# Optimization experiments

Measured on AMD Instinct MI355X. Metric: run time of the kernel, lower is better.

Reference implementation:

```python
import jax, jax.numpy as jnp
import numpy as np

D, H, K, L, F, G, M, OUT = 1280, 16, 80, 4, 5120, 48, 2, 2048
HALF = K // 2  # rotary half dim = 40


def _token_coords(grid_thw, merge_size, N):
    tpi = grid_thw[:, 0] * grid_thw[:, 1] * grid_thw[:, 2]
    cu = jnp.concatenate([jnp.zeros(1, jnp.int32), jnp.cumsum(tpi).astype(jnp.int32)])
    tok = jnp.arange(N, dtype=jnp.int32)
    img_id = jnp.searchsorted(cu[1:], tok, side='right')
    local = tok - cu[img_id]
    h = grid_thw[img_id, 1]
    w = grid_thw[img_id, 2]
    spatial = local % (h * w)
    msq = merge_size * merge_size
    mw = w // merge_size
    group, intra = spatial // msq, spatial % msq
    row = (group // mw) * merge_size + intra // merge_size
    col = (group % mw) * merge_size + intra % merge_size
    return row, col, h, w, cu


def _layernorm(x, s, b, eps=1e-6):
    mu = jnp.mean(x, -1, keepdims=True)
    var = jnp.mean(jnp.square(x - mu), -1, keepdims=True)
    return (x - mu) * jax.lax.rsqrt(var + eps) * s + b


def _rotate_half(x):
    x1, x2 = x[..., :HALF], x[..., HALF:]
    return jnp.concatenate([-x2, x1], axis=-1)


def setup_inputs() -> dict:
    key = jax.random.key(0)
    ks = jax.random.split(key, 16)
    s = 0.02
    inp = {
        'pixels': jax.random.normal(ks[0], (2048, 1536), jnp.float32),
        'grid_thw': jnp.array([[1, 16, 32]] * 4, jnp.int32),
        'pos_embed': jax.random.normal(ks[1], (G * G, D), jnp.float32) * s,
        'patch_w': jax.random.normal(ks[2], (1536, D), jnp.float32) * s,
        'patch_b': jnp.zeros((D,), jnp.float32),
        'ln1_s': jnp.ones((L, D), jnp.float32), 'ln1_b': jnp.zeros((L, D), jnp.float32),
        'qkv_w': jax.random.normal(ks[3], (L, D, 3 * D), jnp.float32) * s,
        'qkv_b': jnp.zeros((L, 3 * D), jnp.float32),
        'proj_w': jax.random.normal(ks[4], (L, D, D), jnp.float32) * s,
        'proj_b': jnp.zeros((L, D), jnp.float32),
        'ln2_s': jnp.ones((L, D), jnp.float32), 'ln2_b': jnp.zeros((L, D), jnp.float32),
        'fc1_w': jax.random.normal(ks[5], (L, D, F), jnp.float32) * s,
        'fc1_b': jnp.zeros((L, F), jnp.float32),
        'fc2_w': jax.random.normal(ks[6], (L, F, D), jnp.float32) * s,
        'fc2_b': jnp.zeros((L, D), jnp.float32),
        'm_norm_s': jnp.ones((D,), jnp.float32), 'm_norm_b': jnp.zeros((D,), jnp.float32),
        'm_fc1_w': jax.random.normal(ks[7], (D * M * M, D * M * M), jnp.float32) * s,
        'm_fc1_b': jnp.zeros((D * M * M,), jnp.float32),
        'm_fc2_w': jax.random.normal(ks[8], (D * M * M, OUT), jnp.float32) * s,
        'm_fc2_b': jnp.zeros((OUT,), jnp.float32),
    }
    return inp


def _forward(pixels, grid_thw, pos_embed, patch_w, patch_b, ln1_s, ln1_b, qkv_w, qkv_b,
             proj_w, proj_b, ln2_s, ln2_b, fc1_w, fc1_b, fc2_w, fc2_b,
             m_norm_s, m_norm_b, m_fc1_w, m_fc1_b, m_fc2_w, m_fc2_b):
    N = pixels.shape[0]
    row, col, h, w, cu = _token_coords(grid_thw, M, N)

    # patch embed: conv with stride==kernel over flattened patches == linear
    x = pixels @ patch_w + patch_b  # [N, D]

    # bilinear position-embedding interpolation onto each image's (h, w) grid
    rf = jnp.where(h > 1, row.astype(jnp.float32) * (G - 1) / jnp.maximum(h - 1, 1), 0.0)
    cf = jnp.where(w > 1, col.astype(jnp.float32) * (G - 1) / jnp.maximum(w - 1, 1), 0.0)
    r0 = jnp.floor(rf).astype(jnp.int32); r1 = jnp.minimum(r0 + 1, G - 1)
    c0 = jnp.floor(cf).astype(jnp.int32); c1 = jnp.minimum(c0 + 1, G - 1)
    wr = (rf - r0)[:, None]; wc = (cf - c0)[:, None]
    pe = (pos_embed[r0 * G + c0] * (1 - wr) * (1 - wc)
          + pos_embed[r0 * G + c1] * (1 - wr) * wc
          + pos_embed[r1 * G + c0] * wr * (1 - wc)
          + pos_embed[r1 * G + c1] * wr * wc)
    x = x + pe

    # 2-D rotary embeddings
    inv_freq = 1.0 / (10000.0 ** (jnp.arange(0, HALF, 2, dtype=jnp.float32) / HALF))
    freqs = jnp.concatenate([row[:, None].astype(jnp.float32) * inv_freq,
                             col[:, None].astype(jnp.float32) * inv_freq], axis=-1)  # [N, HALF]
    emb = jnp.concatenate([freqs, freqs], axis=-1)  # [N, K]
    cos, sin = jnp.cos(emb)[:, None, :], jnp.sin(emb)[:, None, :]  # [N,1,K]

    # block-diagonal segment mask via cu_seqlens (N is a multiple of 128; no pad)
    tok = jnp.arange(N)
    seg = jnp.searchsorted(cu[1:], tok, side='right')
    k_start = cu[jnp.minimum(seg, cu.shape[0] - 2)]
    k_end = cu[jnp.minimum(seg + 1, cu.shape[0] - 1)]
    mask = (tok[None, :] >= k_start[:, None]) & (tok[None, :] < k_end[:, None])  # [N,N]
    scale = K ** -0.5

    for l in range(L):
        hdn = _layernorm(x, ln1_s[l], ln1_b[l])
        qkv = (hdn @ qkv_w[l] + qkv_b[l]).reshape(N, 3, H, K)
        q, k, v = qkv[:, 0], qkv[:, 1], qkv[:, 2]
        q = q * cos + _rotate_half(q) * sin
        k = k * cos + _rotate_half(k) * sin
        scores = jnp.einsum('nhk,mhk->hnm', q, k) * scale
        scores = jnp.where(mask[None], scores, jnp.finfo(scores.dtype).min)
        attn = jax.nn.softmax(scores, axis=-1)
        o = jnp.einsum('hnm,mhk->nhk', attn, v).reshape(N, D)
        x = x + o @ proj_w[l] + proj_b[l]

        hdn = _layernorm(x, ln2_s[l], ln2_b[l])
        ff = jax.nn.gelu(hdn @ fc1_w[l] + fc1_b[l], approximate=True)
        x = x + ff @ fc2_w[l] + fc2_b[l]

    # patch merger
    normed = _layernorm(x, m_norm_s, m_norm_b).reshape(N // (M * M), D * M * M)
    ff = jax.nn.gelu(normed @ m_fc1_w + m_fc1_b, approximate=True)
    return ff @ m_fc2_w + m_fc2_b  # [N/4, OUT]


def reference(pixels, grid_thw, pos_embed, patch_w, patch_b, ln1_s, ln1_b, qkv_w, qkv_b,
              proj_w, proj_b, ln2_s, ln2_b, fc1_w, fc1_b, fc2_w, fc2_b,
              m_norm_s, m_norm_b, m_fc1_w, m_fc1_b, m_fc2_w, m_fc2_b):
    return _forward(pixels, grid_thw, pos_embed, patch_w, patch_b, ln1_s, ln1_b, qkv_w, qkv_b,
                    proj_w, proj_b, ln2_s, ln2_b, fc1_w, fc1_b, fc2_w, fc2_b,
                    m_norm_s, m_norm_b, m_fc1_w, m_fc1_b, m_fc2_w, m_fc2_b)
```

## Files before the change

kernel.cpp:

```cpp
#include <hip/hip_runtime.h>
#include <math.h>

#define DMODEL 1280
#define NHEADS 16
#define FDIM   5120
#define GPOS   48
#define SEG    512

typedef __attribute__((ext_vector_type(8))) short bf16x8;
typedef __attribute__((ext_vector_type(4))) float f32x4;
typedef unsigned short u16;

__device__ __forceinline__ u16 f2bf(float f) {
  unsigned int u = __float_as_uint(f);
  u = (u + 0x7FFFu + ((u >> 16) & 1u)) >> 16;
  return (u16)u;
}
__device__ __forceinline__ float bf2f(u16 u) {
  return __uint_as_float((unsigned int)u << 16);
}
__device__ __forceinline__ float gelu_tanh(float x) {
  float u = 0.7978845608028654f * (x + 0.044715f * x * x * x);
  float t = __expf(2.f * u);
  float th = 1.f - 2.f / (t + 1.f);
  return 0.5f * x * (1.f + th);
}

typedef const __attribute__((address_space(1))) unsigned int* gas_t;
typedef __attribute__((address_space(3))) unsigned int* las_t;
__device__ __forceinline__ void async16(const void* g, void* l) {
  __builtin_amdgcn_global_load_lds((gas_t)g, (las_t)l, 16, 0, 0);
}

#define STG256(mat, PW, ldx, h, kk, pp)                          \
  do {                                                           \
    const u16* g_ = (PW) + (long long)(h) * 128 * (ldx) + (kk);  \
    async16(g_, &L[pp][mat][h][(w * 2 + 0) * 512]);              \
    async16(g_ + 32, &L[pp][mat][h][(w * 2 + 1) * 512]);         \
  } while (0)

#define MM256(ii, ff)                                                          \
  acc[ii][ff] = __builtin_amdgcn_mfma_f32_16x16x32_bf16(aR[(ii) & 3][0],       \
                    bR[ff][0], acc[ii][ff], 0, 0, 0);                          \
  acc[ii][ff] = __builtin_amdgcn_mfma_f32_16x16x32_bf16(aR[(ii) & 3][1],       \
                    bR[ff][1], acc[ii][ff], 0, 0, 0);

#define BAR256() asm volatile("s_barrier" ::: "memory")
#define LGKM0() asm volatile("s_waitcnt lgkmcnt(0)" ::: "memory")

template <int EPI>
__global__ __launch_bounds__(512, 2) void gemm256(
    const u16* __restrict__ A, const u16* __restrict__ B,
    const float* __restrict__ bias, void* __restrict__ Cv,
    int Kd, int lda, int ldb, int ldc, int nsplit, long long pstride) {
  __shared__ __align__(16) u16 L[2][2][2][8192];
  const int sp = blockIdx.z;
  const int Ks = Kd / nsplit;
  const int NT = Ks >> 6;
  const u16* Ab = A + (long long)sp * Ks;
  const u16* Bb = B + (long long)sp * Ks;
  const int m0 = blockIdx.x * 256, n0 = blockIdx.y * 256;
  const int t = threadIdx.x, ln = t & 63, w = t >> 6;
  const int wr = w >> 2, wc = w & 3;
  const int m16 = ln & 15, q = ln >> 4;
  const int r16 = ln >> 2;
  const int csw = (ln & 3) ^ ((ln >> 5) << 1);
  const int rbase = m16 * 32 + (q ^ ((m16 >> 3) << 1)) * 8;

  const u16* Aw = Ab + (long long)(m0 + w * 16 + r16) * lda + csw * 8;
  const u16* Bw = Bb + (long long)(n0 + w * 16 + r16) * ldb + csw * 8;

  f32x4 acc[8][4];
#pragma unroll
  for (int i = 0; i < 8; i++)
#pragma unroll
    for (int j = 0; j < 4; j++)
#pragma unroll
      for (int r = 0; r < 4; r++) acc[i][j][r] = 0.f;

  STG256(0, Aw, lda, 0, 0, 0);
  STG256(0, Aw, lda, 1, 0, 0);
  STG256(1, Bw, ldb, 0, 0, 0);
  STG256(1, Bw, ldb, 1, 0, 0);
  if (NT > 1) {
    STG256(1, Bw, ldb, 0, 64, 1);
    STG256(1, Bw, ldb, 1, 64, 1);
    asm volatile("s_waitcnt vmcnt(4)" ::: "memory");
  } else {
    asm volatile("s_waitcnt vmcnt(0)" ::: "memory");
  }
  BAR256();

  const int wb = (wc & 1) * 4;
  for (int tt = 0; tt < NT; ++tt) {
    const int p = tt & 1;
    const u16* Abuf = &L[p][0][wr][0];
    const u16* Bbuf = &L[p][1][wc >> 1][0];
    bf16x8 aR[4][2], bR[4][2];

#pragma unroll
    for (int i = 0; i < 4; ++i) {
      aR[i][0] = *(const bf16x8*)(Abuf + (i * 2 + 0) * 512 + rbase);
      aR[i][1] = *(const bf16x8*)(Abuf + (i * 2 + 1) * 512 + rbase);
    }
#pragma unroll
    for (int fc = 0; fc < 2; ++fc) {
      bR[fc][0] = *(const bf16x8*)(Bbuf + ((wb + fc) * 2 + 0) * 512 + rbase);
      bR[fc][1] = *(const bf16x8*)(Bbuf + ((wb + fc) * 2 + 1) * 512 + rbase);
    }
    if (tt + 1 < NT) STG256(0, Aw, lda, 0, (tt + 1) * 64, (tt + 1) & 1);
    BAR256();
    LGKM0();
    __builtin_amdgcn_s_setprio(1);
#pragma unroll
    for (int i = 0; i < 4; ++i) { MM256(i, 0); MM256(i, 1); }
    __builtin_amdgcn_s_setprio(0);
    BAR256();

#pragma unroll
    for (int fc = 2; fc < 4; ++fc) {
      bR[fc][0] = *(const bf16x8*)(Bbuf + ((wb + fc) * 2 + 0) * 512 + rbase);
      bR[fc][1] = *(const bf16x8*)(Bbuf + ((wb + fc) * 2 + 1) * 512 + rbase);
    }
    if (tt + 1 < NT) STG256(0, Aw, lda, 1, (tt + 1) * 64, (tt + 1) & 1);
    BAR256();
    LGKM0();
    __builtin_amdgcn_s_setprio(1);
#pragma unroll
    for (int i = 0; i < 4; ++i) { MM256(i, 2); MM256(i, 3); }
    __builtin_amdgcn_s_setprio(0);
    BAR256();

#pragma unroll
    for (int i = 0; i < 4; ++i) {
      aR[i][0] = *(const bf16x8*)(Abuf + ((4 + i) * 2 + 0) * 512 + rbase);
      aR[i][1] = *(const bf16x8*)(Abuf + ((4 + i) * 2 + 1) * 512 + rbase);
    }
    if (tt + 2 < NT) STG256(1, Bw, ldb, 0, (tt + 2) * 64, p);
    BAR256();
    LGKM0();
    __builtin_amdgcn_s_setprio(1);
#pragma unroll
    for (int i = 0; i < 4; ++i) { MM256(4 + i, 2); MM256(4 + i, 3); }
    __builtin_amdgcn_s_setprio(0);
    BAR256();

    if (tt + 2 < NT) STG256(1, Bw, ldb, 1, (tt + 2) * 64, p);
    BAR256();
    LGKM0();
    __builtin_amdgcn_s_setprio(1);
#pragma unroll
    for (int i = 0; i < 4; ++i) { MM256(4 + i, 0); MM256(4 + i, 1); }
    __builtin_amdgcn_s_setprio(0);
    if (tt + 1 < NT) {
      if (tt + 2 < NT) asm volatile("s_waitcnt vmcnt(4)" ::: "memory");
      else             asm volatile("s_waitcnt vmcnt(0)" ::: "memory");
    }
    BAR256();
  }

#pragma unroll
  for (int fr = 0; fr < 8; fr++) {
#pragma unroll
    for (int r = 0; r < 4; r++) {
      int row = m0 + wr * 128 + fr * 16 + q * 4 + r;
      if (EPI == 0) {
        u16* Cp = (u16*)Cv + (long long)sp * pstride + (long long)row * ldc;
#pragma unroll
        for (int fc = 0; fc < 4; fc++)
          Cp[n0 + wc * 64 + fc * 16 + m16] = f2bf(acc[fr][fc][r]);
      } else if (EPI == 1) {
        u16* Cb = (u16*)Cv + (long long)row * ldc;
#pragma unroll
        for (int fc = 0; fc < 4; fc++) {
          int col = n0 + wc * 64 + fc * 16 + m16;
          Cb[col] = f2bf(acc[fr][fc][r] + bias[col]);
        }
      } else {
        u16* Cb = (u16*)Cv + (long long)row * ldc;
#pragma unroll
        for (int fc = 0; fc < 4; fc++) {
          int col = n0 + wc * 64 + fc * 16 + m16;
          Cb[col] = f2bf(gelu_tanh(acc[fr][fc][r] + bias[col]));
        }
      }
    }
  }
}

__global__ __launch_bounds__(256) void fattn_k(
    const u16* __restrict__ qr, const u16* __restrict__ kr,
    const u16* __restrict__ vpT, u16* __restrict__ o, int N, float iscale) {
  __shared__ __align__(16) u16 Ks[2][24][512];
  __shared__ __align__(16) u16 Vs[2][20][512];
  __shared__ __align__(16) u16 Ps[4][32 * 128];
  const int nseg = N >> 9;
  const int hb = blockIdx.y;
  const int h = hb / nseg, seg = hb - h * nseg;
  const int t = threadIdx.x, ln = t & 63, w = t >> 6;
  const int m16 = ln & 15, qh = ln >> 4;
  const int r4 = ln >> 2, gsw = (ln & 3) ^ ((ln >> 5) << 1);
  const int rbase = m16 * 32 + ((qh ^ ((m16 >> 3) << 1)) << 3);
  const long long hN = (long long)h * N;
  const int segbase = seg * SEG;
  const int q0 = segbase + blockIdx.x * 128 + w * 32;

  bf16x8 qf[2][3];
#pragma unroll
  for (int mi = 0; mi < 2; mi++)
#pragma unroll
    for (int ks = 0; ks < 3; ks++)
      qf[mi][ks] = *(const bf16x8*)&qr[(hN + q0 + mi * 16 + m16) * 96 + ks * 32 + qh * 8];

  f32x4 ao[2][5];
#pragma unroll
  for (int mi = 0; mi < 2; mi++)
#pragma unroll
    for (int df = 0; df < 5; df++)
#pragma unroll
      for (int r = 0; r < 4; r++) ao[mi][df][r] = 0.f;
  float m_[2][4], l_[2][4];
#pragma unroll
  for (int mi = 0; mi < 2; mi++)
#pragma unroll
    for (int r = 0; r < 4; r++) { m_[mi][r] = -1e30f; l_[mi][r] = 0.f; }

  auto stage = [&](int c, int pb) {
#pragma unroll
    for (int i = 0; i < 6; i++) {
      int sK = w * 6 + i, f = sK / 3, kg = sK - f * 3;
      async16(&kr[(hN + segbase + c * 128 + f * 16 + r4) * 96 + kg * 32 + gsw * 8],
              &Ks[pb][sK][0]);
    }
#pragma unroll
    for (int i = 0; i < 5; i++) {
      int sV = w * 5 + i, df = sV >> 2, kvg = sV & 3;
      async16(&vpT[((long long)hb * 128 + df * 16 + r4) * SEG + c * 128 + kvg * 32 + gsw * 8],
              &Vs[pb][sV][0]);
    }
  };

  stage(0, 0);
  u16* Pmy = &Ps[w][0];
  for (int c = 0; c < 4; c++) {
    const int pb = c & 1;
    __syncthreads();
    if (c < 3) stage(c + 1, pb ^ 1);

    f32x4 s[2][8];
#pragma unroll
    for (int mi = 0; mi < 2; mi++)
#pragma unroll
      for (int f = 0; f < 8; f++)
#pragma unroll
        for (int r = 0; r < 4; r++) s[mi][f][r] = 0.f;
#pragma unroll
    for (int ks = 0; ks < 3; ks++) {
#pragma unroll
      for (int f = 0; f < 8; f++) {
        bf16x8 kf = *(const bf16x8*)&Ks[pb][f * 3 + ks][rbase];
#pragma unroll
        for (int mi = 0; mi < 2; mi++)
          s[mi][f] = __builtin_amdgcn_mfma_f32_16x16x32_bf16(qf[mi][ks], kf, s[mi][f], 0, 0, 0);
      }
    }

#pragma unroll
    for (int mi = 0; mi < 2; mi++) {
#pragma unroll
      for (int r = 0; r < 4; r++) {
        float mx = s[mi][0][r];
#pragma unroll
        for (int f = 1; f < 8; f++) mx = fmaxf(mx, s[mi][f][r]);
        mx *= iscale;
#pragma unroll
        for (int o2 = 1; o2 <= 8; o2 <<= 1) mx = fmaxf(mx, __shfl_xor(mx, o2));
        float mn = fmaxf(m_[mi][r], mx);
        float corr = __expf(m_[mi][r] - mn);
        m_[mi][r] = mn;
        float rs = 0.f;
#pragma unroll
        for (int f = 0; f < 8; f++) {
          float p = __expf(s[mi][f][r] * iscale - mn);
          s[mi][f][r] = p;
          rs += p;
        }
#pragma unroll
        for (int o2 = 1; o2 <= 8; o2 <<= 1) rs += __shfl_xor(rs, o2);
        l_[mi][r] = l_[mi][r] * corr + rs;
#pragma unroll
        for (int df = 0; df < 5; df++) ao[mi][df][r] *= corr;
      }
    }

#pragma unroll
    for (int mi = 0; mi < 2; mi++) {
#pragma unroll
      for (int r = 0; r < 4; r++) {
        int qq = mi * 16 + qh * 4 + r;
        int base = qq * 128 + (m16 & 7);
        int ql = qq & 7;
#pragma unroll
        for (int f = 0; f < 8; f++) {
          int gr = (f * 2 + (m16 >> 3)) ^ ql;
          Pmy[base + gr * 8] = f2bf(s[mi][f][r]);
        }
      }
    }

#pragma unroll
    for (int ks = 0; ks < 4; ks++) {
      bf16x8 pf[2];
#pragma unroll
      for (int mi = 0; mi < 2; mi++)
        pf[mi] = *(const bf16x8*)&Pmy[(mi * 16 + m16) * 128 +
                                      (((ks * 4 + qh) ^ (m16 & 7)) << 3)];
#pragma unroll
      for (int df = 0; df < 5; df++) {
        bf16x8 vf = *(const bf16x8*)&Vs[pb][df * 4 + ks][rbase];
#pragma unroll
        for (int mi = 0; mi < 2; mi++)
          ao[mi][df] = __builtin_amdgcn_mfma_f32_16x16x32_bf16(pf[mi], vf, ao[mi][df], 0, 0, 0);
      }
    }
  }

#pragma unroll
  for (int mi = 0; mi < 2; mi++) {
#pragma unroll
    for (int r = 0; r < 4; r++) {
      float rl = 1.f / l_[mi][r];
      long long rowb = (long long)(q0 + mi * 16 + qh * 4 + r) * DMODEL + h * 80;
#pragma unroll
      for (int df = 0; df < 5; df++)
        o[rowb + df * 16 + m16] = f2bf(ao[mi][df][r] * rl);
    }
  }
}

template <int S, int RES, int GELU, int OUTBF>
__global__ void reduce_k(const u16* __restrict__ Pp, long long mn, int Nn,
                         const float* __restrict__ bias,
                         const float* __restrict__ res, void* __restrict__ out) {
  long long i = ((long long)blockIdx.x * 256 + threadIdx.x) * 4;
  if (i >= mn) return;
  float vx = 0.f, vy = 0.f, vz = 0.f, vw = 0.f;
#pragma unroll
  for (int s = 0; s < S; s++) {
    ushort4 u4 = *(const ushort4*)(Pp + (long long)s * mn + i);
    vx += bf2f(u4.x); vy += bf2f(u4.y); vz += bf2f(u4.z); vw += bf2f(u4.w);
  }
  int col = (int)(i % Nn);
  vx += bias[col]; vy += bias[col + 1]; vz += bias[col + 2]; vw += bias[col + 3];
  if (GELU) {
    vx = gelu_tanh(vx); vy = gelu_tanh(vy);
    vz = gelu_tanh(vz); vw = gelu_tanh(vw);
  }
  if (RES) {
    float4 r4 = *(const float4*)(res + i);
    vx += r4.x; vy += r4.y; vz += r4.z; vw += r4.w;
  }
  if (OUTBF) {
    ushort4 o; o.x = f2bf(vx); o.y = f2bf(vy); o.z = f2bf(vz); o.w = f2bf(vw);
    *(ushort4*)((u16*)out + i) = o;
  } else {
    float4 o; o.x = vx; o.y = vy; o.z = vz; o.w = vw;
    *(float4*)((float*)out + i) = o;
  }
}

template <int S>
__global__ void redln_k(const u16* __restrict__ Pp, long long mn,
                        const float* __restrict__ bias,
                        float* __restrict__ x,
                        const float* __restrict__ s, const float* __restrict__ b,
                        u16* __restrict__ h) {
  int row = blockIdx.x;
  int d = threadIdx.x * 4;
  long long base = (long long)row * DMODEL + d;
  float vx = 0.f, vy = 0.f, vz = 0.f, vw = 0.f;
#pragma unroll
  for (int si = 0; si < S; si++) {
    ushort4 u4 = *(const ushort4*)(Pp + (long long)si * mn + base);
    vx += bf2f(u4.x); vy += bf2f(u4.y); vz += bf2f(u4.z); vw += bf2f(u4.w);
  }
  vx += bias[d]; vy += bias[d + 1]; vz += bias[d + 2]; vw += bias[d + 3];
  float4 r4 = *(const float4*)(x + base);
  vx += r4.x; vy += r4.y; vz += r4.z; vw += r4.w;
  float4 xv; xv.x = vx; xv.y = vy; xv.z = vz; xv.w = vw;
  *(float4*)(x + base) = xv;
  float sum = vx + vy + vz + vw;
#pragma unroll
  for (int o = 32; o; o >>= 1) sum += __shfl_xor(sum, o);
  __shared__ float red[8];
  int wv = threadIdx.x >> 6, lnn = threadIdx.x & 63;
  if (lnn == 0) red[wv] = sum;
  __syncthreads();
  float mu = 0.f;
  for (int i = 0; i < 5; i++) mu += red[i];
  mu *= (1.f / DMODEL);
  float dx = vx - mu, dy = vy - mu, dz = vz - mu, dw = vw - mu;
  float s2 = dx * dx + dy * dy + dz * dz + dw * dw;
#pragma unroll
  for (int o = 32; o; o >>= 1) s2 += __shfl_xor(s2, o);
  __syncthreads();
  if (lnn == 0) red[wv] = s2;
  __syncthreads();
  float var = 0.f;
  for (int i = 0; i < 5; i++) var += red[i];
  var *= (1.f / DMODEL);
  float rs = rsqrtf(var + 1e-6f);
  ushort4 o4;
  o4.x = f2bf(dx * rs * s[d] + b[d]);
  o4.y = f2bf(dy * rs * s[d + 1] + b[d + 1]);
  o4.z = f2bf(dz * rs * s[d + 2] + b[d + 2]);
  o4.w = f2bf(dw * rs * s[d + 3] + b[d + 3]);
  *(ushort4*)(h + base) = o4;
}

__global__ void wconv_k(const float* __restrict__ in, u16* __restrict__ out,
                        int K, int N) {
  __shared__ float tl[32][33];
  int n0 = blockIdx.x * 32, k0 = blockIdx.y * 32;
  int t = threadIdx.x;
  int r = t >> 5, c = t & 31;
#pragma unroll
  for (int i = 0; i < 4; i++)
    tl[r + 8 * i][c] = in[(long long)(k0 + r + 8 * i) * N + n0 + c];
  __syncthreads();
  int n = t >> 4, kp = (t & 15) * 2;
#pragma unroll
  for (int i = 0; i < 2; i++) {
    ushort2 o;
    o.x = f2bf(tl[kp][n + 16 * i]);
    o.y = f2bf(tl[kp + 1][n + 16 * i]);
    *(ushort2*)&out[(long long)(n0 + n + 16 * i) * K + k0 + kp] = o;
  }
}

__global__ void conv_k(const float* __restrict__ in, u16* __restrict__ out,
                       long long n) {
  long long i = ((long long)blockIdx.x * 256 + threadIdx.x) * 4;
  if (i >= n) return;
  float4 v = *(const float4*)(in + i);
  ushort4 o; o.x = f2bf(v.x); o.y = f2bf(v.y); o.z = f2bf(v.z); o.w = f2bf(v.w);
  *(ushort4*)&out[i] = o;
}

union U16x8 { uint4 v; u16 s[8]; };
__global__ void vtr_k(const u16* __restrict__ in, u16* __restrict__ out) {
  __shared__ u16 tl[64][65];
  int b = blockIdx.z;
  int m0 = blockIdx.x * 64;
  int d0 = blockIdx.y * 64;
  const u16* ib = in + (long long)b * SEG * 128;
  u16* ob = out + (long long)b * 128 * SEG;
  int t = threadIdx.x;
  int r = t >> 3, c8 = (t & 7) * 8;
#pragma unroll
  for (int i = 0; i < 2; i++) {
    U16x8 ld;
    ld.v = *(const uint4*)&ib[(long long)(m0 + r + 32 * i) * 128 + d0 + c8];
#pragma unroll
    for (int j = 0; j < 8; j++) tl[r + 32 * i][c8 + j] = ld.s[j];
  }
  __syncthreads();
  int d = t >> 3, m8 = (t & 7) * 8;
#pragma unroll
  for (int i = 0; i < 2; i++) {
    int dd = d + 32 * i;
    U16x8 st;
#pragma unroll
    for (int j = 0; j < 8; j++) st.s[j] = tl[m8 + j][dd];
    *(uint4*)&ob[(long long)(d0 + dd) * SEG + m0 + m8] = st.v;
  }
}

__global__ void coords_k(const int* __restrict__ g, int nimg,
                         int* __restrict__ rw, int* __restrict__ cl,
                         int* __restrict__ hh, int* __restrict__ ww, int N) {
  int t = blockIdx.x * 256 + threadIdx.x;
  if (t >= N) return;
  int c = 0, local = 0, H = 1, W = 1;
  for (int i = 0; i < nimg; i++) {
    int tpi = g[i * 3] * g[i * 3 + 1] * g[i * 3 + 2];
    if (t >= c && t < c + tpi) { local = t - c; H = g[i * 3 + 1]; W = g[i * 3 + 2]; }
    c += tpi;
  }
  int hw = H * W;
  int sp = local % hw;
  int mw = W >> 1;
  int gr = sp >> 2, intra = sp & 3;
  rw[t] = (gr / mw) * 2 + (intra >> 1);
  cl[t] = (gr % mw) * 2 + (intra & 1);
  hh[t] = H; ww[t] = W;
}

__global__ void peadd_k(float* __restrict__ x, const float* __restrict__ pe,
                        const int* __restrict__ rw, const int* __restrict__ cl,
                        const int* __restrict__ hh, const int* __restrict__ ww) {
  int n = blockIdx.x;
  int d = threadIdx.x * 4;
  int H = hh[n], W = ww[n];
  float rf = (H > 1) ? (float)rw[n] * (float)(GPOS - 1) / (float)(H - 1) : 0.f;
  float cf = (W > 1) ? (float)cl[n] * (float)(GPOS - 1) / (float)(W - 1) : 0.f;
  int r0 = (int)floorf(rf), c0 = (int)floorf(cf);
  int r1 = min(r0 + 1, GPOS - 1), c1 = min(c0 + 1, GPOS - 1);
  float wr = rf - (float)r0, wc = cf - (float)c0;
  float w00 = (1.f - wr) * (1.f - wc), w01 = (1.f - wr) * wc;
  float w10 = wr * (1.f - wc), w11 = wr * wc;
  float4 v00 = *(const float4*)(pe + (long long)(r0 * GPOS + c0) * DMODEL + d);
  float4 v01 = *(const float4*)(pe + (long long)(r0 * GPOS + c1) * DMODEL + d);
  float4 v10 = *(const float4*)(pe + (long long)(r1 * GPOS + c0) * DMODEL + d);
  float4 v11 = *(const float4*)(pe + (long long)(r1 * GPOS + c1) * DMODEL + d);
  float4 xv = *(float4*)(x + (long long)n * DMODEL + d);
  xv.x += w00 * v00.x + w01 * v01.x + w10 * v10.x + w11 * v11.x;
  xv.y += w00 * v00.y + w01 * v01.y + w10 * v10.y + w11 * v11.y;
  xv.z += w00 * v00.z + w01 * v01.z + w10 * v10.z + w11 * v11.z;
  xv.w += w00 * v00.w + w01 * v01.w + w10 * v10.w + w11 * v11.w;
  *(float4*)(x + (long long)n * DMODEL + d) = xv;
}

__global__ void ln_k(const float* __restrict__ X, u16* __restrict__ Y,
                     const float* __restrict__ s, const float* __restrict__ b) {
  int row = blockIdx.x;
  int d = threadIdx.x * 4;
  const float* x = X + (long long)row * DMODEL;
  float4 v = *(const float4*)(x + d);
  float sum = v.x + v.y + v.z + v.w;
#pragma unroll
  for (int o = 32; o; o >>= 1) sum += __shfl_xor(sum, o);
  __shared__ float red[8];
  int wv = threadIdx.x >> 6, lnn = threadIdx.x & 63;
  if (lnn == 0) red[wv] = sum;
  __syncthreads();
  float mu = 0.f;
  for (int i = 0; i < 5; i++) mu += red[i];
  mu *= (1.f / DMODEL);
  float dx = v.x - mu, dy = v.y - mu, dz = v.z - mu, dw = v.w - mu;
  float s2 = dx * dx + dy * dy + dz * dz + dw * dw;
#pragma unroll
  for (int o = 32; o; o >>= 1) s2 += __shfl_xor(s2, o);
  __syncthreads();
  if (lnn == 0) red[wv] = s2;
  __syncthreads();
  float var = 0.f;
  for (int i = 0; i < 5; i++) var += red[i];
  var *= (1.f / DMODEL);
  float rs = rsqrtf(var + 1e-6f);
  ushort4 o4;
  o4.x = f2bf(dx * rs * s[d] + b[d]);
  o4.y = f2bf(dy * rs * s[d + 1] + b[d + 1]);
  o4.z = f2bf(dz * rs * s[d + 2] + b[d + 2]);
  o4.w = f2bf(dw * rs * s[d + 3] + b[d + 3]);
  *(ushort4*)(Y + (long long)row * DMODEL + d) = o4;
}

__global__ void rope_k(const u16* __restrict__ qkv, const int* __restrict__ rw,
                       const int* __restrict__ cl, u16* __restrict__ qr,
                       u16* __restrict__ kr, u16* __restrict__ vp, int N) {
  int n = blockIdx.x, h = blockIdx.y, t = threadIdx.x;
  const u16* src = qkv + (long long)n * (3 * DMODEL) + h * 80;
  long long ob96 = ((long long)h * N + n) * 96;
  long long ob128 = ((long long)h * N + n) * 128;
  if (t < 40) {
    float pos = (t < 20) ? (float)rw[n] : (float)cl[n];
    float infr = exp2f(-13.287712379549449f * (float)(t % 20) * 0.05f);
    float f = pos * infr;
    float cs = cosf(f), sn = sinf(f);
    float q0 = bf2f(src[t]), q1 = bf2f(src[t + 40]);
    qr[ob96 + t] = f2bf(q0 * cs - q1 * sn);
    qr[ob96 + t + 40] = f2bf(q1 * cs + q0 * sn);
    float k0 = bf2f(src[DMODEL + t]), k1 = bf2f(src[DMODEL + t + 40]);
    kr[ob96 + t] = f2bf(k0 * cs - k1 * sn);
    kr[ob96 + t + 40] = f2bf(k1 * cs + k0 * sn);
    vp[ob128 + t] = src[2 * DMODEL + t];
    vp[ob128 + t + 40] = src[2 * DMODEL + t + 40];
  } else {
    int u = t - 40;
    if (u < 16) { qr[ob96 + 80 + u] = 0; kr[ob96 + 80 + u] = 0; }
    vp[ob128 + 80 + u] = 0;
    vp[ob128 + 104 + u] = 0;
  }
}

static void gemm_big(hipStream_t st, int epi, const u16* A, const u16* B,
                     const float* bias, void* C, int M, int Nn, int Kd,
                     int lda, int ldb, int ldc, int nsplit) {
  dim3 g(M / 256, Nn / 256, nsplit), blk(512);
  long long ps = (long long)M * Nn;
  switch (epi) {
    case 0: gemm256<0><<<g, blk, 0, st>>>(A, B, bias, C, Kd, lda, ldb, ldc, nsplit, ps); break;
    case 1: gemm256<1><<<g, blk, 0, st>>>(A, B, bias, C, Kd, lda, ldb, ldc, nsplit, ps); break;
    default: gemm256<3><<<g, blk, 0, st>>>(A, B, bias, C, Kd, lda, ldb, ldc, nsplit, ps); break;
  }
}

extern "C" void kernel_launch(void* const* d_in, const int* in_sizes, int n_in,
                              void* d_out, int out_size, void* d_ws, size_t ws_size,
                              hipStream_t stream) {
  const float* pixels = (const float*)d_in[0];
  const int* grid_thw = (const int*)d_in[1];
  const float* pos_embed = (const float*)d_in[2];
  const float* patch_w = (const float*)d_in[3];
  const float* patch_b = (const float*)d_in[4];
  const float* ln1_s = (const float*)d_in[5];
  const float* ln1_b = (const float*)d_in[6];
  const float* qkv_w = (const float*)d_in[7];
  const float* qkv_b = (const float*)d_in[8];
  const float* proj_w = (const float*)d_in[9];
  const float* proj_b = (const float*)d_in[10];
  const float* ln2_s = (const float*)d_in[11];
  const float* ln2_b = (const float*)d_in[12];
  const float* fc1_w = (const float*)d_in[13];
  const float* fc1_b = (const float*)d_in[14];
  const float* fc2_w = (const float*)d_in[15];
  const float* fc2_b = (const float*)d_in[16];
  const float* mns = (const float*)d_in[17];
  const float* mnb = (const float*)d_in[18];
  const float* mf1w = (const float*)d_in[19];
  const float* mf1b = (const float*)d_in[20];
  const float* mf2w = (const float*)d_in[21];
  const float* mf2b = (const float*)d_in[22];
  float* out = (float*)d_out;

  const int N = in_sizes[0] / 1536;
  const int nimg = in_sizes[1] / 3;
  const int nseg = N / SEG;
  const int nb = NHEADS * nseg;

  char* w = (char*)d_ws;
  size_t off = 0;
  auto alloc = [&](size_t bytes) -> void* {
    void* p = w + off;
    off += (bytes + 255) & ~(size_t)255;
    return p;
  };
  int* rw = (int*)alloc((size_t)N * 4);
  int* cl = (int*)alloc((size_t)N * 4);
  int* hh = (int*)alloc((size_t)N * 4);
  int* ww = (int*)alloc((size_t)N * 4);
  float* x = (float*)alloc((size_t)N * DMODEL * 4);
  u16* h = (u16*)alloc((size_t)N * DMODEL * 2);
  u16* pixbf = (u16*)alloc((size_t)N * 1536 * 2);
  u16* patchT = (u16*)alloc((size_t)DMODEL * 1536 * 2);
  u16* qkvT = (u16*)alloc((size_t)3 * DMODEL * DMODEL * 2);
  u16* projT = (u16*)alloc((size_t)DMODEL * DMODEL * 2);
  u16* fc1T = (u16*)alloc((size_t)FDIM * DMODEL * 2);
  u16* fc2T = (u16*)alloc((size_t)DMODEL * FDIM * 2);
  u16* qkvb = (u16*)alloc((size_t)N * 3 * DMODEL * 2);
  u16* qr = (u16*)alloc((size_t)NHEADS * N * 96 * 2);
  u16* kr = (u16*)alloc((size_t)NHEADS * N * 96 * 2);
  u16* vp = (u16*)alloc((size_t)NHEADS * N * 128 * 2);
  u16* vpT = (u16*)alloc((size_t)NHEADS * N * 128 * 2);
  u16* pad0 = (u16*)alloc((size_t)nb * 2 * SEG * 128 * 2);
  u16* o = (u16*)alloc((size_t)N * DMODEL * 2);
  float* bigA = (float*)alloc((size_t)nb * SEG * SEG * 4);
  float* bigB = (float*)alloc((size_t)nb * SEG * SEG * 2);
  (void)ws_size; (void)pad0;
  u16* mfc1T = qkvb;
  u16* mfc2T = pixbf;
  u16* ffb = (u16*)bigA;
  u16* mf = (u16*)bigA;
  u16* part = (u16*)bigB;
  u16* partA = (u16*)bigA + (size_t)11 * 1024 * 1024;

  const float iscale = 0.11180339887498949f;
  const long long mnD = (long long)N * DMODEL;

  coords_k<<<dim3((N + 255) / 256), 256, 0, stream>>>(grid_thw, nimg, rw, cl, hh, ww, N);
  conv_k<<<dim3((int)(((long long)N * 1536 / 4 + 255) / 256)), 256, 0, stream>>>(
      pixels, pixbf, (long long)N * 1536);
  wconv_k<<<dim3(DMODEL / 32, 1536 / 32), 256, 0, stream>>>(patch_w, patchT, 1536, DMODEL);
  gemm_big(stream, 0, pixbf, patchT, nullptr, part, N, DMODEL, 1536, 1536, 1536,
           DMODEL, 4);
  reduce_k<4, 0, 0, 0><<<dim3((int)((mnD / 4 + 255) / 256)), 256, 0, stream>>>(
      part, mnD, DMODEL, patch_b, nullptr, x);
  peadd_k<<<dim3(N), 320, 0, stream>>>(x, pos_embed, rw, cl, hh, ww);
  ln_k<<<dim3(N), 320, 0, stream>>>(x, h, ln1_s, ln1_b);

  for (int l = 0; l < 4; l++) {
    wconv_k<<<dim3(3 * DMODEL / 32, DMODEL / 32), 256, 0, stream>>>(
        qkv_w + (size_t)l * DMODEL * 3 * DMODEL, qkvT, DMODEL, 3 * DMODEL);
    wconv_k<<<dim3(DMODEL / 32, DMODEL / 32), 256, 0, stream>>>(
        proj_w + (size_t)l * DMODEL * DMODEL, projT, DMODEL, DMODEL);
    wconv_k<<<dim3(FDIM / 32, DMODEL / 32), 256, 0, stream>>>(
        fc1_w + (size_t)l * DMODEL * FDIM, fc1T, DMODEL, FDIM);
    wconv_k<<<dim3(DMODEL / 32, FDIM / 32), 256, 0, stream>>>(
        fc2_w + (size_t)l * FDIM * DMODEL, fc2T, FDIM, DMODEL);

    gemm_big(stream, 0, h, qkvT, nullptr, part, N, 3 * DMODEL, DMODEL,
             DMODEL, DMODEL, 3 * DMODEL, 2);
    reduce_k<2, 0, 0, 1><<<dim3((int)(((long long)N * 3 * DMODEL / 4 + 255) / 256)), 256, 0, stream>>>(
        part, (long long)N * 3 * DMODEL, 3 * DMODEL,
        qkv_b + (size_t)l * 3 * DMODEL, nullptr, qkvb);
    rope_k<<<dim3(N, NHEADS), 64, 0, stream>>>(qkvb, rw, cl, qr, kr, vp, N);
    vtr_k<<<dim3(8, 2, nb), 256, 0, stream>>>(vp, vpT);
    fattn_k<<<dim3(SEG / 128, nb), 256, 0, stream>>>(qr, kr, vpT, o, N, iscale);
    gemm_big(stream, 0, o, projT, nullptr, part, N, DMODEL, DMODEL, DMODEL,
             DMODEL, DMODEL, 4);
    redln_k<4><<<dim3(N), 320, 0, stream>>>(part, mnD, proj_b + (size_t)l * DMODEL,
                                            x, ln2_s + (size_t)l * DMODEL,
                                            ln2_b + (size_t)l * DMODEL, h);
    gemm_big(stream, 0, h, fc1T, nullptr, partA, N, FDIM, DMODEL,
             DMODEL, DMODEL, FDIM, 2);
    reduce_k<2, 0, 1, 1><<<dim3((int)(((long long)N * FDIM / 4 + 255) / 256)), 256, 0, stream>>>(
        partA, (long long)N * FDIM, FDIM, fc1_b + (size_t)l * FDIM, nullptr, ffb);
    gemm_big(stream, 0, ffb, fc2T, nullptr, partA, N, DMODEL, FDIM, FDIM, FDIM,
             DMODEL, 8);
    const float* nsl = (l < 3) ? ln1_s + (size_t)(l + 1) * DMODEL : mns;
    const float* nbl = (l < 3) ? ln1_b + (size_t)(l + 1) * DMODEL : mnb;
    redln_k<8><<<dim3(N), 320, 0, stream>>>(partA, mnD, fc2_b + (size_t)l * DMODEL,
                                            x, nsl, nbl, h);
  }

  const int Mm = N / 4;
  wconv_k<<<dim3(FDIM / 32, FDIM / 32), 256, 0, stream>>>(mf1w, mfc1T, FDIM, FDIM);
  gemm_big(stream, 0, h, mfc1T, nullptr, partA, Mm, FDIM, FDIM, FDIM, FDIM, FDIM, 8);
  reduce_k<8, 0, 1, 1><<<dim3((int)(((long long)Mm * FDIM / 4 + 255) / 256)), 256, 0, stream>>>(
      partA, (long long)Mm * FDIM, FDIM, mf1b, nullptr, mf);
  wconv_k<<<dim3(2048 / 32, FDIM / 32), 256, 0, stream>>>(mf2w, mfc2T, FDIM, 2048);
  gemm_big(stream, 0, mf, mfc2T, nullptr, part, Mm, 2048, FDIM, FDIM, FDIM, 2048, 16);
  reduce_k<16, 0, 0, 0><<<dim3((int)(((long long)Mm * 2048 / 4 + 255) / 256)), 256, 0, stream>>>(
      part, (long long)Mm * 2048, 2048, mf2b, nullptr, out);
}
```

Baseline: 1.518 ms.

## Fuse bias epilogues into GEMMs, drop split-K for QKV/FC1, remap blocks across XCDs

```diff
diff --git a/kernel.cpp b/kernel.cpp
--- a/kernel.cpp
+++ b/kernel.cpp
@@ -30,6 +30,11 @@
 typedef __attribute__((address_space(3))) unsigned int* las_t;
 __device__ __forceinline__ void async16(const void* g, void* l) {
   __builtin_amdgcn_global_load_lds((gas_t)g, (las_t)l, 16, 0, 0);
+}
+
+__device__ __forceinline__ int xcd_remap(int b, int nwg) {
+  int q = nwg >> 3, r = nwg & 7, x = b & 7, d = b >> 3;
+  return (x < r ? x * (q + 1) : r * (q + 1) + (x - r) * q) + d;
 }
 
 #define STG256(mat, PW, ldx, h, kk, pp)                          \
@@ -59,7 +64,9 @@
   const int NT = Ks >> 6;
   const u16* Ab = A + (long long)sp * Ks;
   const u16* Bb = B + (long long)sp * Ks;
-  const int m0 = blockIdx.x * 256, n0 = blockIdx.y * 256;
+  const int gx = gridDim.x;
+  const int lg = xcd_remap(blockIdx.x + gx * blockIdx.y, gx * gridDim.y);
+  const int m0 = (lg % gx) * 256, n0 = (lg / gx) * 256;
   const int t = threadIdx.x, ln = t & 63, w = t >> 6;
   const int wr = w >> 2, wc = w & 3;
   const int m16 = ln & 15, q = ln >> 4;
@@ -195,7 +202,9 @@
   __shared__ __align__(16) u16 Vs[2][20][512];
   __shared__ __align__(16) u16 Ps[4][32 * 128];
   const int nseg = N >> 9;
-  const int hb = blockIdx.y;
+  const int gx = gridDim.x;
+  const int lg = xcd_remap(blockIdx.x + gx * blockIdx.y, gx * gridDim.y);
+  const int strip = lg % gx, hb = lg / gx;
   const int h = hb / nseg, seg = hb - h * nseg;
   const int t = threadIdx.x, ln = t & 63, w = t >> 6;
   const int m16 = ln & 15, qh = ln >> 4;
@@ -203,7 +212,7 @@
   const int rbase = m16 * 32 + ((qh ^ ((m16 >> 3) << 1)) << 3);
   const long long hN = (long long)h * N;
   const int segbase = seg * SEG;
-  const int q0 = segbase + blockIdx.x * 128 + w * 32;
+  const int q0 = segbase + strip * 128 + w * 32;
 
   bf16x8 qf[2][3];
 #pragma unroll
@@ -663,7 +672,6 @@
   u16* ffb = (u16*)bigA;
   u16* mf = (u16*)bigA;
   u16* part = (u16*)bigB;
-  u16* partA = (u16*)bigA + (size_t)11 * 1024 * 1024;
 
   const float iscale = 0.11180339887498949f;
   const long long mnD = (long long)N * DMODEL;
@@ -689,11 +697,8 @@
     wconv_k<<<dim3(DMODEL / 32, FDIM / 32), 256, 0, stream>>>(
         fc2_w + (size_t)l * FDIM * DMODEL, fc2T, FDIM, DMODEL);
 
-    gemm_big(stream, 0, h, qkvT, nullptr, part, N, 3 * DMODEL, DMODEL,
-             DMODEL, DMODEL, 3 * DMODEL, 2);
-    reduce_k<2, 0, 0, 1><<<dim3((int)(((long long)N * 3 * DMODEL / 4 + 255) / 256)), 256, 0, stream>>>(
-        part, (long long)N * 3 * DMODEL, 3 * DMODEL,
-        qkv_b + (size_t)l * 3 * DMODEL, nullptr, qkvb);
+    gemm_big(stream, 1, h, qkvT, qkv_b + (size_t)l * 3 * DMODEL, qkvb, N,
+             3 * DMODEL, DMODEL, DMODEL, DMODEL, 3 * DMODEL, 1);
     rope_k<<<dim3(N, NHEADS), 64, 0, stream>>>(qkvb, rw, cl, qr, kr, vp, N);
     vtr_k<<<dim3(8, 2, nb), 256, 0, stream>>>(vp, vpT);
     fattn_k<<<dim3(SEG / 128, nb), 256, 0, stream>>>(qr, kr, vpT, o, N, iscale);
@@ -702,23 +707,21 @@
     redln_k<4><<<dim3(N), 320, 0, stream>>>(part, mnD, proj_b + (size_t)l * DMODEL,
                                             x, ln2_s + (size_t)l * DMODEL,
                                             ln2_b + (size_t)l * DMODEL, h);
-    gemm_big(stream, 0, h, fc1T, nullptr, partA, N, FDIM, DMODEL,
-             DMODEL, DMODEL, FDIM, 2);
-    reduce_k<2, 0, 1, 1><<<dim3((int)(((long long)N * FDIM / 4 + 255) / 256)), 256, 0, stream>>>(
-        partA, (long long)N * FDIM, FDIM, fc1_b + (size_t)l * FDIM, nullptr, ffb);
-    gemm_big(stream, 0, ffb, fc2T, nullptr, partA, N, DMODEL, FDIM, FDIM, FDIM,
-             DMODEL, 8);
+    gemm_big(stream, 3, h, fc1T, fc1_b + (size_t)l * FDIM, ffb, N, FDIM, DMODEL,
+             DMODEL, DMODEL, FDIM, 1);
+    gemm_big(stream, 0, ffb, fc2T, nullptr, part, N, DMODEL, FDIM, FDIM, FDIM,
+             DMODEL, 4);
     const float* nsl = (l < 3) ? ln1_s + (size_t)(l + 1) * DMODEL : mns;
     const float* nbl = (l < 3) ? ln1_b + (size_t)(l + 1) * DMODEL : mnb;
-    redln_k<8><<<dim3(N), 320, 0, stream>>>(partA, mnD, fc2_b + (size_t)l * DMODEL,
+    redln_k<4><<<dim3(N), 320, 0, stream>>>(part, mnD, fc2_b + (size_t)l * DMODEL,
                                             x, nsl, nbl, h);
   }
 
   const int Mm = N / 4;
   wconv_k<<<dim3(FDIM / 32, FDIM / 32), 256, 0, stream>>>(mf1w, mfc1T, FDIM, FDIM);
-  gemm_big(stream, 0, h, mfc1T, nullptr, partA, Mm, FDIM, FDIM, FDIM, FDIM, FDIM, 8);
-  reduce_k<8, 0, 1, 1><<<dim3((int)(((long long)Mm * FDIM / 4 + 255) / 256)), 256, 0, stream>>>(
-      partA, (long long)Mm * FDIM, FDIM, mf1b, nullptr, mf);
+  gemm_big(stream, 0, h, mfc1T, nullptr, part, Mm, FDIM, FDIM, FDIM, FDIM, FDIM, 4);
+  reduce_k<4, 0, 1, 1><<<dim3((int)(((long long)Mm * FDIM / 4 + 255) / 256)), 256, 0, stream>>>(
+      part, (long long)Mm * FDIM, FDIM, mf1b, nullptr, mf);
   wconv_k<<<dim3(2048 / 32, FDIM / 32), 256, 0, stream>>>(mf2w, mfc2T, FDIM, 2048);
   gemm_big(stream, 0, mf, mfc2T, nullptr, part, Mm, 2048, FDIM, FDIM, FDIM, 2048, 16);
   reduce_k<16, 0, 0, 0><<<dim3((int)(((long long)Mm * 2048 / 4 + 255) / 256)), 256, 0, stream>>>(
```

Measured after the change: 1.441 ms. -5.1%, faster.
